# Performance work log

Measured on AMD Instinct MI355X. Metric: run time of the kernel, lower is better.

## Reference

```python
import jax, jax.numpy as jnp
import numpy as np

CUTOFF = 4.0
RBF_N = 32          # distance_embedding_size == D_rbf
F_DIM = 128         # hidden_size
N_ATOMS = 20000
N_PROBES = 100000
N_EDGES = 262144
LN_EPS = 1e-5


def setup_inputs() -> dict:
    key = jax.random.key(0)
    ks = jax.random.split(key, 20)
    s = 0.02
    inp = {
        "diff_pi": jax.random.normal(ks[0], (N_EDGES, 3), jnp.float32),
        "S_JK": jax.random.normal(ks[1], (N_ATOMS, F_DIM), jnp.float32),
        "V_JK": jax.random.normal(ks[2], (N_ATOMS, 3, F_DIM), jnp.float32),
        "atom_idx": jax.random.randint(ks[3], (N_EDGES,), 0, N_ATOMS),
        "probe_idx": jax.random.randint(ks[4], (N_EDGES,), 0, N_PROBES),
        "num_probes": N_PROBES,
        # state branch params
        "w_s1": jax.random.normal(ks[5], (3 * F_DIM, F_DIM), jnp.float32) * s,
        "b_s1": jnp.zeros((F_DIM,), jnp.float32),
        "g_ln": jnp.ones((F_DIM,), jnp.float32),
        "b_ln": jnp.zeros((F_DIM,), jnp.float32),
        "w_s2": jax.random.normal(ks[6], (F_DIM, F_DIM), jnp.float32) * s,
        "b_s2": jnp.zeros((F_DIM,), jnp.float32),
        # filter branch params
        "w_f1": jax.random.normal(ks[7], (RBF_N, F_DIM), jnp.float32) * s,
        "b_f1": jnp.zeros((F_DIM,), jnp.float32),
        "w_f2": jax.random.normal(ks[8], (F_DIM, F_DIM), jnp.float32) * s,
        "b_f2": jnp.zeros((F_DIM,), jnp.float32),
        # output head params
        "w_o1": jax.random.normal(ks[9], (F_DIM, F_DIM // 2), jnp.float32) * s,
        "b_o1": jnp.zeros((F_DIM // 2,), jnp.float32),
        "w_o2": jax.random.normal(ks[10], (F_DIM // 2, 1), jnp.float32) * s,
        "b_o2": jnp.zeros((1,), jnp.float32),
        "final_bias": jnp.array([-6.1], jnp.float32),
    }
    return inp


def reference(diff_pi, S_JK, V_JK, atom_idx, probe_idx, num_probes,
              w_s1, b_s1, g_ln, b_ln, w_s2, b_s2,
              w_f1, b_f1, w_f2, b_f2,
              w_o1, b_o1, w_o2, b_o2, final_bias):
    silu = jax.nn.silu
    # edge distances
    sq = (diff_pi ** 2).sum(-1)                       # [E]
    dist = jnp.sqrt(sq)                               # [E] exact distance
    dist_safe = jnp.sqrt(sq + 1e-8)[:, None]          # [E,1]
    r_hat = diff_pi / dist_safe                       # [E,3]

    # sinc RBF expansion: sin(n*pi*d/cutoff)/d, n=1..RBF_N
    n = jnp.arange(1, RBF_N + 1, dtype=diff_pi.dtype) # [D]
    e_pi = jnp.sin(dist[:, None] * n * (jnp.pi / CUTOFF)) / dist[:, None]  # [E,D]

    # gather atom features to edges
    n_i = jnp.sqrt((V_JK ** 2).sum(1) + 1e-8)         # [N,F]
    n_e = n_i[atom_idx]                               # [E,F]
    V_e = V_JK[atom_idx]                              # [E,3,F]
    q_pi = (V_e * r_hat[:, :, None]).sum(1)           # [E,F]
    S_e = S_JK[atom_idx]                              # [E,F]

    # state branch: Linear -> LayerNorm -> SiLU -> Linear
    h = jnp.concatenate([S_e, n_e, q_pi], axis=-1)    # [E,3F]
    u = h @ w_s1 + b_s1                               # [E,F]
    mu = u.mean(-1, keepdims=True)
    var = ((u - mu) ** 2).mean(-1, keepdims=True)
    u_norm = (u - mu) / jnp.sqrt(var + LN_EPS) * g_ln + b_ln
    state = silu(u_norm) @ w_s2 + b_s2                # [E,F]

    # filter branch (no normalization -> absolute distance scale)
    W = silu(e_pi @ w_f1 + b_f1) @ w_f2 + b_f2        # [E,F]

    # fuse + output head
    m = (silu((W * state) @ w_o1 + b_o1) @ w_o2 + b_o2)[:, 0]  # [E]

    x = dist / CUTOFF
    env = 1.0 - 21.0 * x ** 5 + 35.0 * x ** 6 - 15.0 * x ** 7
    env = jnp.where(dist < CUTOFF, env, jnp.zeros_like(env))
    m_w = m * env

    # scatter-add to probes
    rho = jax.ops.segment_sum(m_w, probe_idx, num_segments=num_probes)
    return rho + final_bias[0]
```

## Files before the change

### kernel.cpp

```cpp
#include <hip/hip_runtime.h>

#define EPB     64
#define E_TOTAL 262144
#define NPROBE  100000
#define N_ATOMS 20000

#define ASTR   136
#define A2_O   0
#define F1_O   8704
#define EPI_O  17408
#define LDS_SH 19968

#define WS1_O  0
#define WS2_O  49152
#define WF1_O  65536
#define WF2_O  69632
#define WO1_O  86016
#define WT_TOT 94208
#define PQ_O   WT_TOT

typedef __attribute__((ext_vector_type(8))) short          short8;
typedef __attribute__((ext_vector_type(8))) unsigned short ushort8;
typedef __attribute__((ext_vector_type(4))) float          floatx4;

#define MFMA16(a, b, c) __builtin_amdgcn_mfma_f32_16x16x32_bf16((a), (b), (c), 0, 0, 0)

__device__ __forceinline__ short f2bf(float x) {
    unsigned u = __builtin_bit_cast(unsigned, x);
    u = (u + 0x7FFFu + ((u >> 16) & 1u)) >> 16;
    return (short)(unsigned short)u;
}
__device__ __forceinline__ unsigned pk2(float lo, float hi) {
    return __builtin_amdgcn_perm(__builtin_bit_cast(unsigned, hi),
                                 __builtin_bit_cast(unsigned, lo), 0x07060302u);
}
__device__ __forceinline__ float bf2f(unsigned short u) {
    return __builtin_bit_cast(float, ((unsigned)u) << 16);
}
__device__ __forceinline__ float silu_f(float x) { return x / (1.0f + __expf(-x)); }

struct F8 { float v[8]; };
__device__ __forceinline__ F8 ld8(const float* __restrict__ p) {
    F8 r;
    const float4 a = *(const float4*)p;
    const float4 b = *(const float4*)(p + 4);
    r.v[0] = a.x; r.v[1] = a.y; r.v[2] = a.z; r.v[3] = a.w;
    r.v[4] = b.x; r.v[5] = b.y; r.v[6] = b.z; r.v[7] = b.w;
    return r;
}

__global__ void cfr_prep_w(const float* __restrict__ w_s1, const float* __restrict__ w_s2,
                           const float* __restrict__ w_f1, const float* __restrict__ w_f2,
                           const float* __restrict__ w_o1,
                           const float* __restrict__ fb, float* __restrict__ out,
                           unsigned short* __restrict__ wt) {
    int i = blockIdx.x * 256 + threadIdx.x;
    if (i < NPROBE) out[i] = fb[0];
    if (i < WT_TOT) {
        float v;
        if (i < WS2_O)      { int n = i / 384, k = i - n * 384;          v = w_s1[k * 128 + n]; }
        else if (i < WF1_O) { int j = i - WS2_O, n = j >> 7, k = j & 127; v = w_s2[k * 128 + n]; }
        else if (i < WF2_O) { int j = i - WF1_O, n = j >> 5, k = j & 31;  v = w_f1[k * 128 + n]; }
        else if (i < WO1_O) { int j = i - WF2_O, n = j >> 7, k = j & 127; v = w_f2[k * 128 + n]; }
        else                { int j = i - WO1_O, n = j >> 7, k = j & 127; v = w_o1[k * 64 + n]; }
        wt[i] = (unsigned short)f2bf(v);
    }
}

__global__ __launch_bounds__(256, 1) void cfr_prep_pq(
    const float* __restrict__ S, const float* __restrict__ V,
    const float* __restrict__ b_s1,
    const unsigned short* __restrict__ wt, unsigned short* __restrict__ pq)
{
    __shared__ __align__(16) unsigned short bufH[64 * 264];
    __shared__ __align__(16) unsigned short bufV[192 * 136];

    const int t    = threadIdx.x;
    const int a0   = blockIdx.x * 64;
    const int wave = t >> 6;
    const int lane = t & 63;
    const int q    = lane >> 4;
    const int c16  = lane & 15;

#pragma unroll
    for (int it = 0; it < 4; ++it) {
        int idx = it * 256 + t;
        int al = idx >> 4, f8 = (idx & 15) * 8;
        int a = a0 + al;
        ushort8 sS, sN, s0, s1, s2;
        if (a < N_ATOMS) {
            F8 s  = ld8(S + a * 128 + f8);
            F8 v0 = ld8(V + a * 384 + f8);
            F8 v1 = ld8(V + a * 384 + 128 + f8);
            F8 v2 = ld8(V + a * 384 + 256 + f8);
#pragma unroll
            for (int j = 0; j < 8; ++j) {
                sS[j] = (unsigned short)f2bf(s.v[j]);
                sN[j] = (unsigned short)f2bf(sqrtf(v0.v[j]*v0.v[j] + v1.v[j]*v1.v[j] + v2.v[j]*v2.v[j] + 1e-8f));
                s0[j] = (unsigned short)f2bf(v0.v[j]);
                s1[j] = (unsigned short)f2bf(v1.v[j]);
                s2[j] = (unsigned short)f2bf(v2.v[j]);
            }
        } else {
#pragma unroll
            for (int j = 0; j < 8; ++j) { sS[j]=0; sN[j]=0; s0[j]=0; s1[j]=0; s2[j]=0; }
        }
        *(ushort8*)&bufH[al * 264 + f8]        = sS;
        *(ushort8*)&bufH[al * 264 + 128 + f8]  = sN;
        *(ushort8*)&bufV[(al) * 136 + f8]       = s0;
        *(ushort8*)&bufV[(64 + al) * 136 + f8]  = s1;
        *(ushort8*)&bufV[(128 + al) * 136 + f8] = s2;
    }
    __syncthreads();

    const floatx4 zero4 = {0.f, 0.f, 0.f, 0.f};
    float bs1c[2];
#pragma unroll
    for (int ni = 0; ni < 2; ++ni) bs1c[ni] = b_s1[wave * 32 + ni * 16 + c16];

    {
        floatx4 pacc[4][2];
#pragma unroll
        for (int mi = 0; mi < 4; ++mi) { pacc[mi][0] = zero4; pacc[mi][1] = zero4; }
#pragma unroll
        for (int kk = 0; kk < 8; ++kk) {
            short8 bfr[2], af[4];
#pragma unroll
            for (int ni = 0; ni < 2; ++ni) {
                int n = wave * 32 + ni * 16 + c16;
                bfr[ni] = *(const short8*)&wt[WS1_O + n * 384 + kk * 32 + q * 8];
            }
#pragma unroll
            for (int mi = 0; mi < 4; ++mi)
                af[mi] = *(const short8*)&bufH[(mi * 16 + c16) * 264 + kk * 32 + q * 8];
#pragma unroll
            for (int mi = 0; mi < 4; ++mi)
#pragma unroll
                for (int ni = 0; ni < 2; ++ni)
                    pacc[mi][ni] = MFMA16(af[mi], bfr[ni], pacc[mi][ni]);
        }
#pragma unroll
        for (int mi = 0; mi < 4; ++mi)
#pragma unroll
            for (int r = 0; r < 4; ++r) {
                int a = a0 + mi * 16 + q * 4 + r;
                if (a < N_ATOMS)
#pragma unroll
                    for (int ni = 0; ni < 2; ++ni) {
                        int col = wave * 32 + ni * 16 + c16;
                        pq[a * 512 + col] = (unsigned short)f2bf(pacc[mi][ni][r] + bs1c[ni]);
                    }
            }
    }

    short8 bq[4][2];
#pragma unroll
    for (int kk = 0; kk < 4; ++kk)
#pragma unroll
        for (int ni = 0; ni < 2; ++ni) {
            int n = wave * 32 + ni * 16 + c16;
            bq[kk][ni] = *(const short8*)&wt[WS1_O + n * 384 + 256 + kk * 32 + q * 8];
        }
#pragma unroll
    for (int d = 0; d < 3; ++d) {
        floatx4 qacc[4][2];
#pragma unroll
        for (int mi = 0; mi < 4; ++mi) { qacc[mi][0] = zero4; qacc[mi][1] = zero4; }
#pragma unroll
        for (int kk = 0; kk < 4; ++kk) {
            short8 af[4];
#pragma unroll
            for (int mi = 0; mi < 4; ++mi)
                af[mi] = *(const short8*)&bufV[(d * 64 + mi * 16 + c16) * 136 + kk * 32 + q * 8];
#pragma unroll
            for (int mi = 0; mi < 4; ++mi)
#pragma unroll
                for (int ni = 0; ni < 2; ++ni)
                    qacc[mi][ni] = MFMA16(af[mi], bq[kk][ni], qacc[mi][ni]);
        }
#pragma unroll
        for (int mi = 0; mi < 4; ++mi)
#pragma unroll
            for (int r = 0; r < 4; ++r) {
                int a = a0 + mi * 16 + q * 4 + r;
                if (a < N_ATOMS)
#pragma unroll
                    for (int ni = 0; ni < 2; ++ni) {
                        int col = wave * 32 + ni * 16 + c16;
                        pq[a * 512 + (1 + d) * 128 + col] = (unsigned short)f2bf(qacc[mi][ni][r]);
                    }
            }
    }
}

__global__ __launch_bounds__(256, 4) void cfr_main(
    const float* __restrict__ diff,
    const int* __restrict__ atom_idx, const int* __restrict__ probe_idx,
    const unsigned short* __restrict__ wt, const unsigned short* __restrict__ pq,
    const float* __restrict__ g_ln, const float* __restrict__ b_ln,
    const float* __restrict__ b_s2, const float* __restrict__ b_f1,
    const float* __restrict__ b_f2, const float* __restrict__ b_o1,
    const float* __restrict__ w_o2, const float* __restrict__ b_o2,
    float* __restrict__ out)
{
    __shared__ __align__(16) unsigned short LDSu[LDS_SH];
    float* mpart = (float*)&LDSu[EPI_O];

    const int t    = threadIdx.x;
    const int e0   = blockIdx.x * EPB;
    const int wave = t >> 6;
    const int lane = t & 63;
    const int q    = lane >> 4;
    const int c16  = lane & 15;
    const floatx4 zero4 = {0.f, 0.f, 0.f, 0.f};

    {
        const int el = t >> 2;
        const int c0 = (t & 3) * 32;
        const int eg = e0 + el;
        const int a  = atom_idx[eg];
        float dx = diff[eg * 3 + 0], dy = diff[eg * 3 + 1], dz = diff[eg * 3 + 2];
        float sq   = dx * dx + dy * dy + dz * dz;
        float dist = sqrtf(sq);
        float rinv = rsqrtf(sq + 1e-8f);
        float rx = dx * rinv, ry = dy * rinv, rz = dz * rinv;

        const ushort8* pqr = (const ushort8*)(pq + a * 512 + c0);
        float u[32];
#pragma unroll
        for (int g = 0; g < 4; ++g) {
            ushort8 v = pqr[g];
#pragma unroll
            for (int j = 0; j < 8; ++j) u[g * 8 + j] = bf2f(v[j]);
        }
#pragma unroll
        for (int g = 0; g < 4; ++g) {
            ushort8 v = pqr[16 + g];
#pragma unroll
            for (int j = 0; j < 8; ++j) u[g * 8 + j] = fmaf(bf2f(v[j]), rx, u[g * 8 + j]);
        }
#pragma unroll
        for (int g = 0; g < 4; ++g) {
            ushort8 v = pqr[32 + g];
#pragma unroll
            for (int j = 0; j < 8; ++j) u[g * 8 + j] = fmaf(bf2f(v[j]), ry, u[g * 8 + j]);
        }
#pragma unroll
        for (int g = 0; g < 4; ++g) {
            ushort8 v = pqr[48 + g];
#pragma unroll
            for (int j = 0; j < 8; ++j) u[g * 8 + j] = fmaf(bf2f(v[j]), rz, u[g * 8 + j]);
        }
        float s = 0.f, s2 = 0.f;
#pragma unroll
        for (int j = 0; j < 32; ++j) { s += u[j]; s2 = fmaf(u[j], u[j], s2); }
        s  += __shfl_xor(s, 1);  s  += __shfl_xor(s, 2);
        s2 += __shfl_xor(s2, 1); s2 += __shfl_xor(s2, 2);
        float mu = s * (1.f / 128.f);
        float rstd = rsqrtf(s2 * (1.f / 128.f) - mu * mu + 1e-5f);
        const float4* gp = (const float4*)(g_ln + c0);
        const float4* bp = (const float4*)(b_ln + c0);
        unsigned pko[16];
#pragma unroll
        for (int g4 = 0; g4 < 8; ++g4) {
            float4 gg = gp[g4], bb = bp[g4];
            float y0 = silu_f((u[g4 * 4 + 0] - mu) * rstd * gg.x + bb.x);
            float y1 = silu_f((u[g4 * 4 + 1] - mu) * rstd * gg.y + bb.y);
            float y2 = silu_f((u[g4 * 4 + 2] - mu) * rstd * gg.z + bb.z);
            float y3 = silu_f((u[g4 * 4 + 3] - mu) * rstd * gg.w + bb.w);
            pko[g4 * 2 + 0] = pk2(y0, y1);
            pko[g4 * 2 + 1] = pk2(y2, y3);
        }
        uint4* dst = (uint4*)&LDSu[A2_O + el * ASTR + c0];
        dst[0] = make_uint4(pko[0], pko[1], pko[2], pko[3]);
        dst[1] = make_uint4(pko[4], pko[5], pko[6], pko[7]);
        dst[2] = make_uint4(pko[8], pko[9], pko[10], pko[11]);
        dst[3] = make_uint4(pko[12], pko[13], pko[14], pko[15]);
        float inv = 1.0f / dist;
        float sv[8];
#pragma unroll
        for (int j = 0; j < 8; ++j) {
            float nf = (float)((t & 3) * 8 + j + 1);
            sv[j] = __sinf(dist * nf * 0.785398163397448f) * inv;
        }
        *(uint4*)&LDSu[EPI_O + el * 40 + (t & 3) * 8] =
            make_uint4(pk2(sv[0], sv[1]), pk2(sv[2], sv[3]), pk2(sv[4], sv[5]), pk2(sv[6], sv[7]));
    }
    __syncthreads();

    {
        short8 ae[4], be[2];
#pragma unroll
        for (int mi = 0; mi < 4; ++mi)
            ae[mi] = *(const short8*)&LDSu[EPI_O + (mi * 16 + c16) * 40 + q * 8];
#pragma unroll
        for (int ni = 0; ni < 2; ++ni) {
            int n = wave * 32 + ni * 16 + c16;
            be[ni] = *(const short8*)&wt[WF1_O + n * 32 + q * 8];
        }
        floatx4 facc[4][2];
#pragma unroll
        for (int mi = 0; mi < 4; ++mi)
#pragma unroll
            for (int ni = 0; ni < 2; ++ni)
                facc[mi][ni] = MFMA16(ae[mi], be[ni], zero4);
        float bf1c[2];
#pragma unroll
        for (int ni = 0; ni < 2; ++ni) bf1c[ni] = b_f1[wave * 32 + ni * 16 + c16];
#pragma unroll
        for (int mi = 0; mi < 4; ++mi)
#pragma unroll
            for (int r = 0; r < 4; ++r) {
                int row = mi * 16 + q * 4 + r;
#pragma unroll
                for (int ni = 0; ni < 2; ++ni) {
                    float v = facc[mi][ni][r] + bf1c[ni];
                    LDSu[F1_O + row * ASTR + (wave * 32 + ni * 16 + c16)] =
                        (unsigned short)(__builtin_bit_cast(unsigned, silu_f(v)) >> 16);
                }
            }
    }
    __syncthreads();

    {
        floatx4 sacc[4][2], wacc[4][2];
#pragma unroll
        for (int mi = 0; mi < 4; ++mi)
#pragma unroll
            for (int ni = 0; ni < 2; ++ni) { sacc[mi][ni] = zero4; wacc[mi][ni] = zero4; }
#pragma unroll
        for (int kk = 0; kk < 4; ++kk) {
            short8 a2f[4], f1f[4], b2[2], bw[2];
#pragma unroll
            for (int ni = 0; ni < 2; ++ni) {
                int n = wave * 32 + ni * 16 + c16;
                b2[ni] = *(const short8*)&wt[WS2_O + n * 128 + kk * 32 + q * 8];
                bw[ni] = *(const short8*)&wt[WF2_O + n * 128 + kk * 32 + q * 8];
            }
#pragma unroll
            for (int mi = 0; mi < 4; ++mi) {
                a2f[mi] = *(const short8*)&LDSu[A2_O + (mi * 16 + c16) * ASTR + kk * 32 + q * 8];
                f1f[mi] = *(const short8*)&LDSu[F1_O + (mi * 16 + c16) * ASTR + kk * 32 + q * 8];
            }
#pragma unroll
            for (int mi = 0; mi < 4; ++mi)
#pragma unroll
                for (int ni = 0; ni < 2; ++ni) {
                    sacc[mi][ni] = MFMA16(a2f[mi], b2[ni], sacc[mi][ni]);
                    wacc[mi][ni] = MFMA16(f1f[mi], bw[ni], wacc[mi][ni]);
                }
        }
        __syncthreads();
        float bs2c[2], bf2c[2];
#pragma unroll
        for (int ni = 0; ni < 2; ++ni) {
            int col = wave * 32 + ni * 16 + c16;
            bs2c[ni] = b_s2[col]; bf2c[ni] = b_f2[col];
        }
#pragma unroll
        for (int mi = 0; mi < 4; ++mi)
#pragma unroll
            for (int r = 0; r < 4; ++r) {
                int row = mi * 16 + q * 4 + r;
#pragma unroll
                for (int ni = 0; ni < 2; ++ni) {
                    float g = (sacc[mi][ni][r] + bs2c[ni]) * (wacc[mi][ni][r] + bf2c[ni]);
                    LDSu[A2_O + row * ASTR + (wave * 32 + ni * 16 + c16)] =
                        (unsigned short)(__builtin_bit_cast(unsigned, g) >> 16);
                }
            }
    }
    __syncthreads();

    {
        const int n2 = wave * 16 + c16;
        floatx4 oacc[4];
#pragma unroll
        for (int mi = 0; mi < 4; ++mi) oacc[mi] = zero4;
#pragma unroll
        for (int kk = 0; kk < 4; ++kk) {
            short8 bfr = *(const short8*)&wt[WO1_O + n2 * 128 + kk * 32 + q * 8];
#pragma unroll
            for (int mi = 0; mi < 4; ++mi) {
                short8 af = *(const short8*)&LDSu[A2_O + (mi * 16 + c16) * ASTR + kk * 32 + q * 8];
                oacc[mi] = MFMA16(af, bfr, oacc[mi]);
            }
        }
        float bo1c = b_o1[n2], wo2c = w_o2[n2];
#pragma unroll
        for (int mi = 0; mi < 4; ++mi)
#pragma unroll
            for (int r = 0; r < 4; ++r) {
                float s = silu_f(oacc[mi][r] + bo1c) * wo2c;
#pragma unroll
                for (int d = 1; d < 16; d <<= 1) s += __shfl_xor(s, d, 64);
                if (c16 == 0) mpart[(mi * 16 + q * 4 + r) * 4 + wave] = s;
            }
    }
    __syncthreads();

    if (t < EPB) {
        int eg = e0 + t;
        float m = mpart[t * 4 + 0] + mpart[t * 4 + 1] + mpart[t * 4 + 2] + mpart[t * 4 + 3] + b_o2[0];
        float dx = diff[eg * 3 + 0], dy = diff[eg * 3 + 1], dz = diff[eg * 3 + 2];
        float dist = sqrtf(dx * dx + dy * dy + dz * dz);
        float x  = dist * 0.25f;
        float x2 = x * x, x4 = x2 * x2;
        float x5 = x4 * x, x6 = x5 * x, x7 = x6 * x;
        float env = 1.0f - 21.0f * x5 + 35.0f * x6 - 15.0f * x7;
        env = (dist < 4.0f) ? env : 0.0f;
        float mw = m * env;
        if (mw != 0.f) unsafeAtomicAdd(&out[probe_idx[eg]], mw);
    }
}

extern "C" void kernel_launch(void* const* d_in, const int* in_sizes, int n_in,
                              void* d_out, int out_size, void* d_ws, size_t ws_size,
                              hipStream_t stream) {
    const float* diff    = (const float*)d_in[0];
    const float* S_JK    = (const float*)d_in[1];
    const float* V_JK    = (const float*)d_in[2];
    const int*   atom_i  = (const int*)d_in[3];
    const int*   probe_i = (const int*)d_in[4];
    const float* w_s1 = (const float*)d_in[6];
    const float* b_s1 = (const float*)d_in[7];
    const float* g_ln = (const float*)d_in[8];
    const float* b_ln = (const float*)d_in[9];
    const float* w_s2 = (const float*)d_in[10];
    const float* b_s2 = (const float*)d_in[11];
    const float* w_f1 = (const float*)d_in[12];
    const float* b_f1 = (const float*)d_in[13];
    const float* w_f2 = (const float*)d_in[14];
    const float* b_f2 = (const float*)d_in[15];
    const float* w_o1 = (const float*)d_in[16];
    const float* b_o1 = (const float*)d_in[17];
    const float* w_o2 = (const float*)d_in[18];
    const float* b_o2 = (const float*)d_in[19];
    const float* fbias = (const float*)d_in[20];
    float* out = (float*)d_out;

    unsigned short* wt = (unsigned short*)d_ws;
    unsigned short* pqp = wt + PQ_O;

    cfr_prep_w<<<(NPROBE + 255) / 256, 256, 0, stream>>>(w_s1, w_s2, w_f1, w_f2, w_o1,
                                                         fbias, out, wt);
    cfr_prep_pq<<<(N_ATOMS + 63) / 64, 256, 0, stream>>>(S_JK, V_JK, b_s1, wt, pqp);
    cfr_main<<<E_TOTAL / EPB, 256, 0, stream>>>(diff, atom_i, probe_i, wt, pqp,
        g_ln, b_ln, b_s2, b_f1, b_f2, b_o1, w_o2, b_o2, out);
}
```

Before: 242.3 us.

## Swizzle prep LDS layout, raise prep occupancy, use fast rcp and hardware sin

Replaces the padded LDS rows in the atom-projection prep kernel with an XOR-swizzled unpadded layout, shrinking shared memory so launch bounds can allow two blocks per CU. In the main edge kernel, SiLU and the RBF 1/d now use the hardware reciprocal instead of a true division. The sinc RBF uses the native sin instruction, which takes its argument in revolutions, so d/8 times n replaces the radian form. The goal is fewer LDS bank conflicts and cheaper transcendental math, at a small accuracy cost from the approximate rcp and sin.

```diff
diff --git a/kernel.cpp b/kernel.cpp
--- a/kernel.cpp
+++ b/kernel.cpp
@@ -37,7 +37,9 @@
 __device__ __forceinline__ float bf2f(unsigned short u) {
     return __builtin_bit_cast(float, ((unsigned)u) << 16);
 }
-__device__ __forceinline__ float silu_f(float x) { return x / (1.0f + __expf(-x)); }
+__device__ __forceinline__ float silu_f(float x) {
+    return x * __builtin_amdgcn_rcpf(1.0f + __expf(-x));
+}
 
 struct F8 { float v[8]; };
 __device__ __forceinline__ F8 ld8(const float* __restrict__ p) {
@@ -67,13 +69,13 @@
     }
 }
 
-__global__ __launch_bounds__(256, 1) void cfr_prep_pq(
+__global__ __launch_bounds__(256, 2) void cfr_prep_pq(
     const float* __restrict__ S, const float* __restrict__ V,
     const float* __restrict__ b_s1,
     const unsigned short* __restrict__ wt, unsigned short* __restrict__ pq)
 {
-    __shared__ __align__(16) unsigned short bufH[64 * 264];
-    __shared__ __align__(16) unsigned short bufV[192 * 136];
+    __shared__ __align__(16) unsigned short bufH[64 * 256];
+    __shared__ __align__(16) unsigned short bufV[192 * 128];
 
     const int t    = threadIdx.x;
     const int a0   = blockIdx.x * 64;
@@ -105,15 +107,19 @@
 #pragma unroll
             for (int j = 0; j < 8; ++j) { sS[j]=0; sN[j]=0; s0[j]=0; s1[j]=0; s2[j]=0; }
         }
-        *(ushort8*)&bufH[al * 264 + f8]        = sS;
-        *(ushort8*)&bufH[al * 264 + 128 + f8]  = sN;
-        *(ushort8*)&bufV[(al) * 136 + f8]       = s0;
-        *(ushort8*)&bufV[(64 + al) * 136 + f8]  = s1;
-        *(ushort8*)&bufV[(128 + al) * 136 + f8] = s2;
+        const unsigned swH = (unsigned)((al & 7) << 4);
+        char* hrow  = (char*)bufH + al * 512;
+        char* vbase = (char*)bufV;
+        *(ushort8*)(hrow + ((f8 * 2) ^ swH))         = sS;
+        *(ushort8*)(hrow + ((256 + f8 * 2) ^ swH))   = sN;
+        *(ushort8*)(vbase + al * 256         + ((f8 * 2) ^ swH)) = s0;
+        *(ushort8*)(vbase + (64 + al) * 256  + ((f8 * 2) ^ swH)) = s1;
+        *(ushort8*)(vbase + (128 + al) * 256 + ((f8 * 2) ^ swH)) = s2;
     }
     __syncthreads();
 
     const floatx4 zero4 = {0.f, 0.f, 0.f, 0.f};
+    const unsigned swr = (unsigned)((c16 & 7) << 4);
     float bs1c[2];
 #pragma unroll
     for (int ni = 0; ni < 2; ++ni) bs1c[ni] = b_s1[wave * 32 + ni * 16 + c16];
@@ -131,8 +137,10 @@
                 bfr[ni] = *(const short8*)&wt[WS1_O + n * 384 + kk * 32 + q * 8];
             }
 #pragma unroll
-            for (int mi = 0; mi < 4; ++mi)
-                af[mi] = *(const short8*)&bufH[(mi * 16 + c16) * 264 + kk * 32 + q * 8];
+            for (int mi = 0; mi < 4; ++mi) {
+                int row = mi * 16 + c16;
+                af[mi] = *(const short8*)((const char*)bufH + row * 512 + ((unsigned)(kk * 64 + q * 16) ^ swr));
+            }
 #pragma unroll
             for (int mi = 0; mi < 4; ++mi)
 #pragma unroll
@@ -170,8 +178,10 @@
         for (int kk = 0; kk < 4; ++kk) {
             short8 af[4];
 #pragma unroll
-            for (int mi = 0; mi < 4; ++mi)
-                af[mi] = *(const short8*)&bufV[(d * 64 + mi * 16 + c16) * 136 + kk * 32 + q * 8];
+            for (int mi = 0; mi < 4; ++mi) {
+                int row = d * 64 + mi * 16 + c16;
+                af[mi] = *(const short8*)((const char*)bufV + row * 256 + ((unsigned)(kk * 64 + q * 16) ^ swr));
+            }
 #pragma unroll
             for (int mi = 0; mi < 4; ++mi)
 #pragma unroll
@@ -276,12 +286,13 @@
         dst[1] = make_uint4(pko[4], pko[5], pko[6], pko[7]);
         dst[2] = make_uint4(pko[8], pko[9], pko[10], pko[11]);
         dst[3] = make_uint4(pko[12], pko[13], pko[14], pko[15]);
-        float inv = 1.0f / dist;
+        float inv = __builtin_amdgcn_rcpf(dist);
+        float d8  = dist * 0.125f;
         float sv[8];
 #pragma unroll
         for (int j = 0; j < 8; ++j) {
             float nf = (float)((t & 3) * 8 + j + 1);
-            sv[j] = __sinf(dist * nf * 0.785398163397448f) * inv;
+            sv[j] = __builtin_amdgcn_sinf(d8 * nf) * inv;
         }
         *(uint4*)&LDSu[EPI_O + el * 40 + (t & 3) * 8] =
             make_uint4(pk2(sv[0], sv[1]), pk2(sv[2], sv[3]), pk2(sv[4], sv[5]), pk2(sv[6], sv[7]));
```

Result: faster. 232.1 us (-4.2%).
